# Optimization experiments

Hardware: AMD Instinct MI355X
Metric: run time of the kernel (lower is better)

## Reference

```python
import jax, jax.numpy as jnp
import numpy as np

B, S, F, H, P = 2048, 168, 7, 128, 96  # batch, window, features, hidden, pred_len


def setup_inputs() -> dict:
    key = jax.random.key(0)
    ks = jax.random.split(key, 16)
    sc = 0.05
    return {
        "xb": jax.random.normal(ks[0], (B, S, F), dtype=jnp.float32),
        # encoder LSTM (1 layer, unidirectional); gate order i,f,g,o like torch
        "W_ih_enc": jax.random.normal(ks[1], (4 * H, F), dtype=jnp.float32) * sc,
        "W_hh_enc": jax.random.normal(ks[2], (4 * H, H), dtype=jnp.float32) * sc,
        "b_ih_enc": jax.random.normal(ks[3], (4 * H,), dtype=jnp.float32) * sc,
        "b_hh_enc": jax.random.normal(ks[4], (4 * H,), dtype=jnp.float32) * sc,
        # attention linear: (H+F) -> S
        "W_att": jax.random.normal(ks[5], (S, H + F), dtype=jnp.float32) * sc,
        "b_att": jax.random.normal(ks[6], (S,), dtype=jnp.float32) * sc,
        # decoder LSTMCell: input_size=H, hidden=H
        "W_ih_dec": jax.random.normal(ks[7], (4 * H, H), dtype=jnp.float32) * sc,
        "W_hh_dec": jax.random.normal(ks[8], (4 * H, H), dtype=jnp.float32) * sc,
        "b_ih_dec": jax.random.normal(ks[9], (4 * H,), dtype=jnp.float32) * sc,
        "b_hh_dec": jax.random.normal(ks[10], (4 * H,), dtype=jnp.float32) * sc,
        # out linear: H -> F
        "W_out": jax.random.normal(ks[11], (F, H), dtype=jnp.float32) * sc,
        "b_out": jax.random.normal(ks[12], (F,), dtype=jnp.float32) * sc,
        # final linear (output_size==1 branch): F -> 1
        "W_fin": jax.random.normal(ks[13], (1, F), dtype=jnp.float32) * sc,
        "b_fin": jax.random.normal(ks[14], (1,), dtype=jnp.float32) * sc,
    }


def _gates(pre):
    i, f, g, o = jnp.split(pre, 4, axis=-1)
    return jax.nn.sigmoid(i), jax.nn.sigmoid(f), jnp.tanh(g), jax.nn.sigmoid(o)


def _forward(xb, W_ih_enc, W_hh_enc, b_ih_enc, b_hh_enc, W_att, b_att,
             W_ih_dec, W_hh_dec, b_ih_dec, b_hh_dec, W_out, b_out, W_fin, b_fin):
    b_enc = b_ih_enc + b_hh_enc
    x_ih = jnp.einsum('bsf,gf->sbg', xb, W_ih_enc)  # precompute input projections [S,B,4H]

    def enc_step(carry, xg):
        h, c = carry
        i, f, g, o = _gates(xg + h @ W_hh_enc.T + b_enc)
        c = f * c + i * g
        h = o * jnp.tanh(c)
        return (h, c), h

    h0 = jnp.zeros((xb.shape[0], W_hh_enc.shape[1]), dtype=xb.dtype)
    (h_T, _), enc_hs = jax.lax.scan(enc_step, (h0, h0), x_ih)
    encoder_output = jnp.transpose(enc_hs, (1, 0, 2))  # [B,S,H]

    b_dec = b_ih_dec + b_hh_dec

    def dec_step(carry, _):
        prev_h, y_prev = carry
        attn_in = jnp.concatenate([prev_h, y_prev], axis=1)          # [B,H+F]
        attn_w = jax.nn.softmax(attn_in @ W_att.T + b_att, axis=-1)  # [B,S]
        combine = jnp.einsum('bs,bsh->bh', attn_w, encoder_output)   # [B,H]
        # torch code: rnn_hidden, rnn_hidden = cell(combine, (prev_h, prev_h))
        # -> the CELL state c' is what survives; h'/output gate discarded.
        i, f, g, _ = _gates(combine @ W_ih_dec.T + prev_h @ W_hh_dec.T + b_dec)
        c_new = f * prev_h + i * g
        out = c_new @ W_out.T + b_out                                # [B,F]
        return (c_new, out), out

    y0 = xb[:, -1, :]
    _, outs = jax.lax.scan(dec_step, (h_T, y0), None, length=P)      # [P,B,F]
    outputs = jnp.transpose(outs, (1, 0, 2))                         # [B,P,F]
    return outputs @ W_fin.T + b_fin                                 # [B,P,1]


def reference(xb, W_ih_enc, W_hh_enc, b_ih_enc, b_hh_enc, W_att, b_att,
              W_ih_dec, W_hh_dec, b_ih_dec, b_hh_dec, W_out, b_out, W_fin, b_fin):
    return _forward(xb, W_ih_enc, W_hh_enc, b_ih_enc, b_hh_enc, W_att, b_att,
                    W_ih_dec, W_hh_dec, b_ih_dec, b_hh_dec, W_out, b_out, W_fin, b_fin)
```

## Files before the change

### kernel.cpp

```cpp
#include <hip/hip_runtime.h>
#include <hip/hip_fp8.h>

#define NB   2048
#define SEQ  168
#define NF   7
#define NH   128
#define NP   96
#define EROWS 8
#define DROWS 8
#define NTHR 512
#define KE   160
#define KD   256
#define HXS  168
#define CTS  264
#define LS4  30

typedef _Float16 h16;
typedef _Float16 h16x8 __attribute__((ext_vector_type(8)));
typedef float    f32x2 __attribute__((ext_vector_type(2)));
typedef float    f32x4 __attribute__((ext_vector_type(4)));
typedef unsigned int u32x4 __attribute__((ext_vector_type(4)));

__device__ __forceinline__ void mfma_av(f32x4& acc, h16x8 a, const h16x8& b_agpr) {
  asm("v_mfma_f32_16x16x32_f16 %0, %1, %2, %0"
      : "+v"(acc) : "v"(a), "a"(b_agpr));
}
#define PIN_A(x) asm volatile("" : "+a"(x))

__device__ __forceinline__ float sigm(float x) { return 1.f / (1.f + __expf(-x)); }
__device__ __forceinline__ float tanh_(float x) {
  float e = __expf(-2.f * fabsf(x));
  return copysignf((1.f - e) / (1.f + e), x);
}

template <bool HI>
__device__ __forceinline__ unsigned int pack2_fp8(float a, float b, unsigned int old) {
#if __has_builtin(__builtin_amdgcn_cvt_pk_fp8_f32)
  return (unsigned int)__builtin_amdgcn_cvt_pk_fp8_f32(a, b, (int)old, HI);
#else
  __hip_fp8_e4m3 qa(a), qb(b);
  unsigned int pair = (unsigned int)(*(unsigned char*)&qa) |
                      ((unsigned int)(*(unsigned char*)&qb) << 8);
  return HI ? ((old & 0x0000ffffu) | (pair << 16)) : ((old & 0xffff0000u) | pair);
#endif
}
template <bool HI>
__device__ __forceinline__ f32x2 unp2(unsigned int w) {
#if __has_builtin(__builtin_amdgcn_cvt_pk_f32_fp8)
  return __builtin_amdgcn_cvt_pk_f32_fp8(w, HI);
#else
  __hip_fp8_e4m3 a, b;
  constexpr unsigned int sh = HI ? 16 : 0;
  *(unsigned char*)&a = (w >> sh) & 0xff;
  *(unsigned char*)&b = (w >> (sh + 8)) & 0xff;
  f32x2 r; r.x = (float)a; r.y = (float)b; return r;
#endif
}

constexpr size_t WENC_OFF   = 0;
constexpr size_t WDEC_OFF   = 163840;
constexpr size_t WEFF_OFF   = 425984;
constexpr size_t BEFF_OFF   = 468992;
constexpr size_t WCOMB_OFF  = 469760;
constexpr size_t BCONST_OFF = 470272;
constexpr size_t BENC_OFF   = 470528;
constexpr size_t BDEC_OFF   = 472576;
constexpr size_t ENC_OFF    = 524288;
constexpr size_t ENC2_OFF   = 31981568;
constexpr size_t HT_OFF     = 44564480;

constexpr int HIST_OFF = 0;
constexpr int CATH_OFF = 122880;
constexpr int ATTW_OFF = 131328;
constexpr int WAT2_OFF = 136704;
constexpr int D0_OFF   = 146944;
constexpr int OUTP_OFF = 152320;
constexpr int YH_OFF   = 152576;
constexpr int DSMEM    = 152832;

__global__ void setup_weights(const float* __restrict__ Wih_enc, const float* __restrict__ Whh_enc,
                              const float* __restrict__ Wih_dec, const float* __restrict__ Whh_dec,
                              const float* __restrict__ Watt, const float* __restrict__ batt,
                              const float* __restrict__ Wout, const float* __restrict__ bout,
                              const float* __restrict__ Wfin, const float* __restrict__ bfin,
                              const float* __restrict__ bihe, const float* __restrict__ bhhe,
                              const float* __restrict__ bihd, const float* __restrict__ bhhd,
                              char* __restrict__ ws) {
  int idx = blockIdx.x * blockDim.x + threadIdx.x;
  constexpr int A0 = 81920;
  constexpr int A1 = A0 + 131072;
  constexpr int A2 = A1 + 21504;
  constexpr int A3 = A2 + 168;
  constexpr int A4 = A3 + 128;
  constexpr int A5 = A4 + 1;
  constexpr int A6 = A5 + 512;
  if (idx < A0) {
    int n = idx / KE, k = idx % KE;
    float v = 0.f;
    if (k < NF) v = Wih_enc[n * NF + k];
    else if (k >= 8 && k < 136) v = Whh_enc[n * NH + (k - 8)];
    ((h16*)(ws + WENC_OFF))[idx] = (h16)v;
  } else if (idx < A1) {
    int i = idx - A0;
    int n = i / KD, k = i % KD;
    float v = (k < NH) ? Wih_dec[n * NH + k] : Whh_dec[n * NH + (k - NH)];
    ((h16*)(ws + WDEC_OFF))[i] = (h16)v;
  } else if (idx < A2) {
    int i = idx - A1;
    int s = i / NH, k = i % NH;
    float v = Watt[s * (NH + NF) + k];
    #pragma unroll
    for (int f = 0; f < NF; ++f)
      v += Watt[s * (NH + NF) + NH + f] * Wout[f * NH + k];
    ((h16*)(ws + WEFF_OFF))[i] = (h16)v;
  } else if (idx < A3) {
    int s = idx - A2;
    float v = batt[s];
    #pragma unroll
    for (int f = 0; f < NF; ++f)
      v += Watt[s * (NH + NF) + NH + f] * bout[f];
    ((float*)(ws + BEFF_OFF))[s] = v;
  } else if (idx < A4) {
    int k = idx - A3;
    float v = 0.f;
    #pragma unroll
    for (int f = 0; f < NF; ++f) v += Wfin[f] * Wout[f * NH + k];
    ((float*)(ws + WCOMB_OFF))[k] = v;
  } else if (idx < A5) {
    float v = bfin[0];
    #pragma unroll
    for (int f = 0; f < NF; ++f) v += bout[f] * Wfin[f];
    ((float*)(ws + BCONST_OFF))[0] = v;
  } else if (idx < A6) {
    int g = idx - A5;
    ((float*)(ws + BENC_OFF))[g] = bihe[g] + bhhe[g];
    ((float*)(ws + BDEC_OFF))[g] = bihd[g] + bhhd[g];
  }
}

__global__ __attribute__((amdgpu_flat_work_group_size(NTHR, NTHR), amdgpu_waves_per_eu(2, 2)))
void enc_kernel(const float* __restrict__ xb, const h16* __restrict__ w16enc,
                const float* __restrict__ bencp, unsigned int* __restrict__ encw,
                unsigned int* __restrict__ encw2, float* __restrict__ hT) {
  __shared__ alignas(16) h16 sh_hx[2][16][HXS];

  const int t  = threadIdx.x;
  const int r0 = blockIdx.x * EROWS;

  for (int i = t; i < 2 * 16 * HXS; i += NTHR) ((h16*)sh_hx)[i] = (h16)0.f;
  __syncthreads();
  if (t < EROWS * NF) {
    int r = t / NF, f = t - (t / NF) * NF;
    sh_hx[0][r][f] = (h16)xb[((size_t)(r0 + r) * SEQ + 0) * NF + f];
  }

  const int w  = t >> 6;
  const int l  = t & 63;
  const int lq = l >> 4;
  const int ln = l & 15;
  const int hcol = w * 16 + ln;
  const int mrow = lq * 4;
  const bool act = (lq < 2);

  const int j  = t & 3;
  const int rf = t >> 2;
  const int xr = rf / NF;
  const int xf = rf - xr * NF;

  h16x8 bfE[4][5];
  float bE[4];
  #pragma unroll
  for (int g = 0; g < 4; ++g) {
    int n = g * 128 + hcol;
    bE[g] = bencp[n];
    #pragma unroll
    for (int kt = 0; kt < 5; ++kt) {
      bfE[g][kt] = *(const h16x8*)(w16enc + n * KE + kt * 32 + lq * 8);
      PIN_A(bfE[g][kt]);
    }
  }

  float creg[4] = {0.f, 0.f, 0.f, 0.f};
  float hlast[4] = {0.f, 0.f, 0.f, 0.f};
  float hprev[4] = {0.f, 0.f, 0.f, 0.f};
  unsigned int hpack[4] = {0u, 0u, 0u, 0u};
  float xstash = 0.f;

  __syncthreads();

  for (int s = 0; s < SEQ; ++s) {
    const int cur = s & 1;
    if ((s & 3) == 0 && t < EROWS * NF * 4) {
      int sx = s + 1 + j;
      xstash = (sx < SEQ) ? xb[((size_t)(r0 + xr) * SEQ + sx) * NF + xf] : 0.f;
    }

    f32x4 ac[4] = {{0.f,0.f,0.f,0.f},{0.f,0.f,0.f,0.f},{0.f,0.f,0.f,0.f},{0.f,0.f,0.f,0.f}};
    #pragma unroll
    for (int kt = 0; kt < 5; ++kt) {
      h16x8 af = *(const h16x8*)(&sh_hx[cur][ln][kt * 32 + lq * 8]);
      #pragma unroll
      for (int g = 0; g < 4; ++g)
        mfma_av(ac[g], af, bfE[g][kt]);
    }

    if (act) {
      #pragma unroll
      for (int reg = 0; reg < 4; ++reg) {
        float gi = sigm(ac[0][reg] + bE[0]);
        float gf = sigm(ac[1][reg] + bE[1]);
        float gg = tanh_(ac[2][reg] + bE[2]);
        float go = sigm(ac[3][reg] + bE[3]);
        float c = gf * creg[reg] + gi * gg;
        creg[reg] = c;
        float h = go * tanh_(c);
        hlast[reg] = h;
        sh_hx[cur ^ 1][mrow + reg][8 + hcol] = (h16)h;
        float hs = h * 16.f;
        if ((s & 1) == 0) hprev[reg] = hs;
        else if ((s & 3) == 1) hpack[reg] = pack2_fp8<false>(hprev[reg], hs, hpack[reg]);
        else                   hpack[reg] = pack2_fp8<true>(hprev[reg], hs, hpack[reg]);
      }
      if ((s & 3) == 3) {
        int s4 = s >> 2;
        if (s4 < LS4) {
          #pragma unroll
          for (int reg = 0; reg < 4; ++reg)
            encw[((size_t)(r0 + mrow + reg) * LS4 + s4) * NH + hcol] = hpack[reg];
        } else {
          int q = s4 - LS4;
          #pragma unroll
          for (int reg = 0; reg < 4; ++reg)
            encw2[(((size_t)(r0 + mrow + reg) * 3 + (q >> 2)) * NH + hcol) * 4 + (q & 3)] = hpack[reg];
        }
      }
    }
    if (t < EROWS * NF * 4 && (s & 3) == j && s + 1 < SEQ)
      sh_hx[cur ^ 1][xr][xf] = (h16)xstash;
    __syncthreads();
  }

  if (act) {
    #pragma unroll
    for (int reg = 0; reg < 4; ++reg)
      hT[(size_t)(r0 + mrow + reg) * NH + hcol] = hlast[reg];
  }
}

__global__ __attribute__((amdgpu_flat_work_group_size(NTHR, NTHR), amdgpu_waves_per_eu(2, 2)))
void dec_kernel(const float* __restrict__ xb, const float* __restrict__ Watt,
                const float* __restrict__ Wout, const float* __restrict__ bout,
                const h16* __restrict__ w16dec, const h16* __restrict__ weff,
                const float* __restrict__ beffp, const float* __restrict__ wcombp,
                const float* __restrict__ bconstp, const float* __restrict__ bdecp,
                const unsigned int* __restrict__ encw, const unsigned int* __restrict__ encw2,
                const float* __restrict__ hT, float* __restrict__ out) {
  extern __shared__ char smem[];
  unsigned int* hist = (unsigned int*)(smem + HIST_OFF);
  h16*   sh_cath  = (h16*)(smem + CATH_OFF);
  float* sh_attw  = (float*)(smem + ATTW_OFF);
  h16*   sh_watt2 = (h16*)(smem + WAT2_OFF);
  float* sh_d0    = (float*)(smem + D0_OFF);
  float* sh_outp  = (float*)(smem + OUTP_OFF);
  float* sh_yh    = (float*)(smem + YH_OFF);

  const int t  = threadIdx.x;
  const int r0 = blockIdx.x * DROWS;

  for (int i = t; i < 2 * 8 * CTS; i += NTHR)   sh_cath[i] = (h16)0.f;
  for (int i = t; i < 40 * NH; i += NTHR)       sh_watt2[i] = weff[128 * NH + i];
  {
    const u32x4* src = (const u32x4*)(encw + (size_t)r0 * LS4 * NH);
    for (int i = t; i < (DROWS * LS4 * NH) / 4; i += NTHR)
      ((u32x4*)hist)[i] = src[i];
  }

  const int w  = t >> 6;
  const int l  = t & 63;
  const int lq = l >> 4;
  const int ln = l & 15;
  const int hcol = w * 16 + ln;
  const bool act = (lq < 2);

  h16x8 bfD[3][8];
  float bD[3];
  #pragma unroll
  for (int g = 0; g < 3; ++g) {
    int n = g * 128 + hcol;
    bD[g] = bdecp[n];
    #pragma unroll
    for (int kt = 0; kt < 8; ++kt) {
      bfD[g][kt] = *(const h16x8*)(w16dec + n * KD + kt * 32 + lq * 8);
      PIN_A(bfD[g][kt]);
    }
  }
  h16x8 bfA[4];
  #pragma unroll
  for (int kt = 0; kt < 4; ++kt) {
    bfA[kt] = *(const h16x8*)(weff + hcol * NH + kt * 32 + lq * 8);
    PIN_A(bfA[kt]);
  }
  const float beffR = beffp[hcol];
  const int s2v = 128 + hcol;
  const float beff2 = (w < 3 && s2v < SEQ) ? beffp[s2v] : 0.f;
  const float wcombR = wcombp[hcol];
  const float bconstv = bconstp[0];

  float creg[4] = {0.f, 0.f, 0.f, 0.f};
  if (act) {
    #pragma unroll
    for (int reg = 0; reg < 4; ++reg) {
      int row = lq * 4 + reg;
      float hv = hT[(size_t)(r0 + row) * NH + hcol];
      creg[reg] = hv;
      sh_cath[0 * 8 * CTS + row * CTS + 128 + hcol] = (h16)hv;
    }
  }
  if (t < DROWS * NF) {
    int r = t / NF, f = t - (t / NF) * NF;
    float a = bout[f];
    const float* wr = Wout + f * NH;
    const float* hp = hT + (size_t)(r0 + r) * NH;
    #pragma unroll 8
    for (int k = 0; k < NH; k += 4) {
      float4 pv = *(const float4*)(hp + k);
      float4 wv = *(const float4*)(wr + k);
      a += pv.x * wv.x + pv.y * wv.y + pv.z * wv.z + pv.w * wv.w;
    }
    sh_yh[t] = a;
  }
  __syncthreads();
  for (int i = t; i < DROWS * SEQ; i += NTHR) {
    int r = i / SEQ, s = i - (i / SEQ) * SEQ;
    float a = 0.f;
    #pragma unroll
    for (int f = 0; f < NF; ++f) {
      float y0f = xb[((size_t)(r0 + r) * SEQ + (SEQ - 1)) * NF + f];
      a += (y0f - sh_yh[r * NF + f]) * Watt[s * (NH + NF) + NH + f];
    }
    sh_d0[i] = a;
  }

  const int dr = t >> 7;
  const int dh = t & 127;
  const unsigned int* hrowA = hist + (size_t)dr * (LS4 * NH) + dh;
  const unsigned int* hrowB = hist + (size_t)(dr + 4) * (LS4 * NH) + dh;
  const float* erowA = sh_attw + dr * SEQ;
  const float* erowB = sh_attw + (dr + 4) * SEQ;

  u32x4 tA[3], tB[3];
  {
    const u32x4* e2 = (const u32x4*)encw2;
    #pragma unroll
    for (int b = 0; b < 3; ++b) {
      tA[b] = e2[((size_t)(r0 + dr)     * 3 + b) * NH + dh];
      tB[b] = e2[((size_t)(r0 + dr + 4) * 3 + b) * NH + dh];
    }
  }
  __syncthreads();

  for (int p = 0; p < NP; ++p) {
    const int CA = p & 1;

    if (p > 0 && t < DROWS) {
      float a = bconstv;
      #pragma unroll
      for (int w2 = 0; w2 < 8; ++w2) a += sh_outp[w2 * 8 + t];
      out[(size_t)(r0 + t) * NP + (p - 1)] = a;
    }

    {
      h16x8 afA[4];
      #pragma unroll
      for (int kt = 0; kt < 4; ++kt)
        afA[kt] = *(const h16x8*)(sh_cath + CA * 8 * CTS + (ln & 7) * CTS + 128 + kt * 32 + lq * 8);
      f32x4 acc = {0.f, 0.f, 0.f, 0.f};
      #pragma unroll
      for (int kt = 0; kt < 4; ++kt)
        mfma_av(acc, afA[kt], bfA[kt]);
      if (act) {
        #pragma unroll
        for (int reg = 0; reg < 4; ++reg) {
          int row = lq * 4 + reg;
          float lg = acc[reg] + beffR;
          if (p == 0) lg += sh_d0[row * SEQ + hcol];
          lg = fminf(fmaxf(lg, -30.f), 30.f);
          sh_attw[row * SEQ + hcol] = __expf(lg);
        }
      }
      if (w < 3) {
        int srow = (s2v < SEQ ? s2v : SEQ - 1) - 128;
        f32x4 acc2 = {0.f, 0.f, 0.f, 0.f};
        #pragma unroll
        for (int kt = 0; kt < 4; ++kt) {
          h16x8 bf2 = *(const h16x8*)(sh_watt2 + srow * NH + kt * 32 + lq * 8);
          acc2 = __builtin_amdgcn_mfma_f32_16x16x32_f16(afA[kt], bf2, acc2, 0, 0, 0);
        }
        if (s2v < SEQ && act) {
          #pragma unroll
          for (int reg = 0; reg < 4; ++reg) {
            int row = lq * 4 + reg;
            float lg = acc2[reg] + beff2;
            if (p == 0) lg += sh_d0[row * SEQ + s2v];
            lg = fminf(fmaxf(lg, -30.f), 30.f);
            sh_attw[row * SEQ + s2v] = __expf(lg);
          }
        }
      }
    }
    __syncthreads();

    {
      float dA = erowA[l] + erowA[64 + l];
      float dB = erowB[l] + erowB[64 + l];
      if (l < SEQ - 128) { dA += erowA[128 + l]; dB += erowB[128 + l]; }
      #pragma unroll
      for (int k = 1; k < 64; k <<= 1) {
        dA += __shfl_xor(dA, k);
        dB += __shfl_xor(dB, k);
      }
      const float invA = 0.0625f / dA;
      const float invB = 0.0625f / dB;

      f32x2 avA = {0.f, 0.f};
      f32x2 avB = {0.f, 0.f};
      #pragma unroll 6
      for (int s4 = 0; s4 < LS4; ++s4) {
        unsigned int evA = hrowA[s4 * NH];
        unsigned int evB = hrowB[s4 * NH];
        float4 eA = *(const float4*)(erowA + s4 * 4);
        float4 eB = *(const float4*)(erowB + s4 * 4);
        f32x2 wA01 = {eA.x, eA.y}, wA23 = {eA.z, eA.w};
        f32x2 wB01 = {eB.x, eB.y}, wB23 = {eB.z, eB.w};
        avA = wA01 * unp2<false>(evA) + avA;
        avA = wA23 * unp2<true>(evA) + avA;
        avB = wB01 * unp2<false>(evB) + avB;
        avB = wB23 * unp2<true>(evB) + avB;
      }
      #pragma unroll
      for (int b = 0; b < 3; ++b) {
        #pragma unroll
        for (int jj = 0; jj < 4; ++jj) {
          int s4 = LS4 + b * 4 + jj;
          unsigned int evA = tA[b][jj];
          unsigned int evB = tB[b][jj];
          float4 eA = *(const float4*)(erowA + s4 * 4);
          float4 eB = *(const float4*)(erowB + s4 * 4);
          f32x2 wA01 = {eA.x, eA.y}, wA23 = {eA.z, eA.w};
          f32x2 wB01 = {eB.x, eB.y}, wB23 = {eB.z, eB.w};
          avA = wA01 * unp2<false>(evA) + avA;
          avA = wA23 * unp2<true>(evA) + avA;
          avB = wB01 * unp2<false>(evB) + avB;
          avB = wB23 * unp2<true>(evB) + avB;
        }
      }
      sh_cath[CA * 8 * CTS + dr * CTS + dh]       = (h16)((avA.x + avA.y) * invA);
      sh_cath[CA * 8 * CTS + (dr + 4) * CTS + dh] = (h16)((avB.x + avB.y) * invB);
    }
    __syncthreads();

    {
      f32x4 ag[3] = {{0.f,0.f,0.f,0.f},{0.f,0.f,0.f,0.f},{0.f,0.f,0.f,0.f}};
      #pragma unroll
      for (int kt = 0; kt < 8; ++kt) {
        h16x8 af = *(const h16x8*)(sh_cath + CA * 8 * CTS + (ln & 7) * CTS + kt * 32 + lq * 8);
        #pragma unroll
        for (int g = 0; g < 3; ++g)
          mfma_av(ag[g], af, bfD[g][kt]);
      }
      if (act) {
        float contrib[4];
        #pragma unroll
        for (int reg = 0; reg < 4; ++reg) {
          int row = lq * 4 + reg;
          float gi = sigm(ag[0][reg] + bD[0]);
          float gf = sigm(ag[1][reg] + bD[1]);
          float gg = tanh_(ag[2][reg] + bD[2]);
          float cn = gf * creg[reg] + gi * gg;
          creg[reg] = cn;
          sh_cath[(CA ^ 1) * 8 * CTS + row * CTS + 128 + hcol] = (h16)cn;
          contrib[reg] = cn * wcombR;
        }
        #pragma unroll
        for (int reg = 0; reg < 4; ++reg) {
          float rsum = contrib[reg];
          rsum += __shfl_xor(rsum, 1);
          rsum += __shfl_xor(rsum, 2);
          rsum += __shfl_xor(rsum, 4);
          rsum += __shfl_xor(rsum, 8);
          if (ln == 0) sh_outp[w * 8 + lq * 4 + reg] = rsum;
        }
      }
    }
    __syncthreads();
  }

  if (t < DROWS) {
    float a = bconstv;
    #pragma unroll
    for (int w2 = 0; w2 < 8; ++w2) a += sh_outp[w2 * 8 + t];
    out[(size_t)(r0 + t) * NP + (NP - 1)] = a;
  }
}

extern "C" void kernel_launch(void* const* d_in, const int* in_sizes, int n_in,
                              void* d_out, int out_size, void* d_ws, size_t ws_size,
                              hipStream_t stream) {
  const float* xb      = (const float*)d_in[0];
  const float* Wih_enc = (const float*)d_in[1];
  const float* Whh_enc = (const float*)d_in[2];
  const float* bih_enc = (const float*)d_in[3];
  const float* bhh_enc = (const float*)d_in[4];
  const float* Watt    = (const float*)d_in[5];
  const float* batt    = (const float*)d_in[6];
  const float* Wih_dec = (const float*)d_in[7];
  const float* Whh_dec = (const float*)d_in[8];
  const float* bih_dec = (const float*)d_in[9];
  const float* bhh_dec = (const float*)d_in[10];
  const float* Wout    = (const float*)d_in[11];
  const float* bout    = (const float*)d_in[12];
  const float* Wfin    = (const float*)d_in[13];
  const float* bfin    = (const float*)d_in[14];
  char* ws = (char*)d_ws;

  hipFuncSetAttribute(reinterpret_cast<const void*>(dec_kernel),
                      hipFuncAttributeMaxDynamicSharedMemorySize, DSMEM);

  setup_weights<<<920, 256, 0, stream>>>(Wih_enc, Whh_enc, Wih_dec, Whh_dec,
                                         Watt, batt, Wout, bout, Wfin, bfin,
                                         bih_enc, bhh_enc, bih_dec, bhh_dec, ws);
  enc_kernel<<<NB / EROWS, NTHR, 0, stream>>>(
      xb, (const h16*)(ws + WENC_OFF), (const float*)(ws + BENC_OFF),
      (unsigned int*)(ws + ENC_OFF), (unsigned int*)(ws + ENC2_OFF),
      (float*)(ws + HT_OFF));
  dec_kernel<<<NB / DROWS, NTHR, DSMEM, stream>>>(
      xb, Watt, Wout, bout,
      (const h16*)(ws + WDEC_OFF), (const h16*)(ws + WEFF_OFF),
      (const float*)(ws + BEFF_OFF), (const float*)(ws + WCOMB_OFF),
      (const float*)(ws + BCONST_OFF), (const float*)(ws + BDEC_OFF),
      (const unsigned int*)(ws + ENC_OFF), (const unsigned int*)(ws + ENC2_OFF),
      (const float*)(ws + HT_OFF), (float*)d_out);
}
```

Measured before the change: 929.1 us.

## Fuse encoder and decoder into one kernel with LDS-resident encoder history

Merges the encoder and decoder kernels into a single kernel per 8-row block. Encoder history is written straight into shared memory instead of a global buffer that the decoder re-reads, and x is preloaded into LDS as fp16. The decoder's hidden-state matmul now runs early, overlapping the attention computation. Softmax denominators come from per-wave partial sums instead of a cross-lane reduction over exp values, and outputs are buffered eight steps at a time before being written. The cost is larger shared memory for the encoder phase, which may lower occupancy, and a longer serial kernel.

```diff
diff --git a/kernel.cpp b/kernel.cpp
--- a/kernel.cpp
+++ b/kernel.cpp
@@ -65,18 +65,22 @@
 constexpr size_t BCONST_OFF = 470272;
 constexpr size_t BENC_OFF   = 470528;
 constexpr size_t BDEC_OFF   = 472576;
-constexpr size_t ENC_OFF    = 524288;
 constexpr size_t ENC2_OFF   = 31981568;
 constexpr size_t HT_OFF     = 44564480;
 
-constexpr int HIST_OFF = 0;
-constexpr int CATH_OFF = 122880;
-constexpr int ATTW_OFF = 131328;
-constexpr int WAT2_OFF = 136704;
-constexpr int D0_OFF   = 146944;
-constexpr int OUTP_OFF = 152320;
-constexpr int YH_OFF   = 152576;
-constexpr int DSMEM    = 152832;
+constexpr int HIST_OFF   = 0;
+constexpr int CATH_OFF   = 122880;
+constexpr int ATTW_OFF   = 131328;
+constexpr int WAT2_OFF   = 136704;
+constexpr int D0_OFF     = 146944;
+constexpr int OUTP_OFF   = 152320;
+constexpr int YH_OFF     = 152576;
+constexpr int DPART_OFF  = 152832;
+constexpr int DPART2_OFF = 153088;
+constexpr int OBUF_OFF   = 153216;
+constexpr int DSMEM      = 153472;
+constexpr int SHHX_OFF = 122880;
+constexpr int X16_OFF  = 133632;
 
 __global__ void setup_weights(const float* __restrict__ Wih_enc, const float* __restrict__ Whh_enc,
                               const float* __restrict__ Wih_dec, const float* __restrict__ Whh_dec,
@@ -139,20 +143,31 @@
 }
 
 __global__ __attribute__((amdgpu_flat_work_group_size(NTHR, NTHR), amdgpu_waves_per_eu(2, 2)))
-void enc_kernel(const float* __restrict__ xb, const h16* __restrict__ w16enc,
-                const float* __restrict__ bencp, unsigned int* __restrict__ encw,
-                unsigned int* __restrict__ encw2, float* __restrict__ hT) {
-  __shared__ alignas(16) h16 sh_hx[2][16][HXS];
+void fused_kernel(const float* __restrict__ xb, const h16* __restrict__ w16enc,
+                  const float* __restrict__ bencp, unsigned int* __restrict__ encw2,
+                  float* __restrict__ hTg,
+                  const float* __restrict__ Watt, const float* __restrict__ Wout,
+                  const float* __restrict__ bout,
+                  const h16* __restrict__ w16dec, const h16* __restrict__ weff,
+                  const float* __restrict__ beffp, const float* __restrict__ wcombp,
+                  const float* __restrict__ bconstp, const float* __restrict__ bdecp,
+                  float* __restrict__ out) {
+  extern __shared__ char smem[];
+  unsigned int* hist = (unsigned int*)(smem + HIST_OFF);
+  h16 (*sh_hx)[16][HXS] = (h16(*)[16][HXS])(smem + SHHX_OFF);
+  h16*   x16      = (h16*)(smem + X16_OFF);
+  h16*   sh_cath  = (h16*)(smem + CATH_OFF);
+  float* sh_attw  = (float*)(smem + ATTW_OFF);
+  h16*   sh_watt2 = (h16*)(smem + WAT2_OFF);
+  float* sh_d0    = (float*)(smem + D0_OFF);
+  float* sh_outp  = (float*)(smem + OUTP_OFF);
+  float* sh_yh    = (float*)(smem + YH_OFF);
+  float* sh_dp    = (float*)(smem + DPART_OFF);
+  float* sh_dp2   = (float*)(smem + DPART2_OFF);
+  float* sh_obuf  = (float*)(smem + OBUF_OFF);
 
   const int t  = threadIdx.x;
   const int r0 = blockIdx.x * EROWS;
-
-  for (int i = t; i < 2 * 16 * HXS; i += NTHR) ((h16*)sh_hx)[i] = (h16)0.f;
-  __syncthreads();
-  if (t < EROWS * NF) {
-    int r = t / NF, f = t - (t / NF) * NF;
-    sh_hx[0][r][f] = (h16)xb[((size_t)(r0 + r) * SEQ + 0) * NF + f];
-  }
 
   const int w  = t >> 6;
   const int l  = t & 63;
@@ -162,10 +177,9 @@
   const int mrow = lq * 4;
   const bool act = (lq < 2);
 
-  const int j  = t & 3;
-  const int rf = t >> 2;
-  const int xr = rf / NF;
-  const int xf = rf - xr * NF;
+  for (int i = t; i < 2 * 16 * HXS; i += NTHR) ((h16*)sh_hx)[i] = (h16)0.f;
+  for (int i = t; i < EROWS * SEQ * NF; i += NTHR)
+    x16[i] = (h16)xb[(size_t)r0 * SEQ * NF + i];
 
   h16x8 bfE[4][5];
   float bE[4];
@@ -179,21 +193,21 @@
       PIN_A(bfE[g][kt]);
     }
   }
+  __syncthreads();
+  if (t < EROWS * NF) {
+    int r = t / NF, f = t - (t / NF) * NF;
+    sh_hx[0][r][f] = x16[(r * SEQ + 0) * NF + f];
+  }
 
   float creg[4] = {0.f, 0.f, 0.f, 0.f};
-  float hlast[4] = {0.f, 0.f, 0.f, 0.f};
+  float hstate[4] = {0.f, 0.f, 0.f, 0.f};
   float hprev[4] = {0.f, 0.f, 0.f, 0.f};
   unsigned int hpack[4] = {0u, 0u, 0u, 0u};
-  float xstash = 0.f;
 
   __syncthreads();
 
   for (int s = 0; s < SEQ; ++s) {
     const int cur = s & 1;
-    if ((s & 3) == 0 && t < EROWS * NF * 4) {
-      int sx = s + 1 + j;
-      xstash = (sx < SEQ) ? xb[((size_t)(r0 + xr) * SEQ + sx) * NF + xf] : 0.f;
-    }
 
     f32x4 ac[4] = {{0.f,0.f,0.f,0.f},{0.f,0.f,0.f,0.f},{0.f,0.f,0.f,0.f},{0.f,0.f,0.f,0.f}};
     #pragma unroll
@@ -214,7 +228,7 @@
         float c = gf * creg[reg] + gi * gg;
         creg[reg] = c;
         float h = go * tanh_(c);
-        hlast[reg] = h;
+        hstate[reg] = h;
         sh_hx[cur ^ 1][mrow + reg][8 + hcol] = (h16)h;
         float hs = h * 16.f;
         if ((s & 1) == 0) hprev[reg] = hs;
@@ -226,7 +240,7 @@
         if (s4 < LS4) {
           #pragma unroll
           for (int reg = 0; reg < 4; ++reg)
-            encw[((size_t)(r0 + mrow + reg) * LS4 + s4) * NH + hcol] = hpack[reg];
+            hist[(size_t)(mrow + reg) * (LS4 * NH) + s4 * NH + hcol] = hpack[reg];
         } else {
           int q = s4 - LS4;
           #pragma unroll
@@ -235,52 +249,23 @@
         }
       }
     }
-    if (t < EROWS * NF * 4 && (s & 3) == j && s + 1 < SEQ)
-      sh_hx[cur ^ 1][xr][xf] = (h16)xstash;
+    if (t < EROWS * NF && s + 1 < SEQ) {
+      int r = t / NF, f = t - (t / NF) * NF;
+      sh_hx[cur ^ 1][r][f] = x16[(r * SEQ + (s + 1)) * NF + f];
+    }
     __syncthreads();
   }
 
   if (act) {
     #pragma unroll
     for (int reg = 0; reg < 4; ++reg)
-      hT[(size_t)(r0 + mrow + reg) * NH + hcol] = hlast[reg];
-  }
-}
-
-__global__ __attribute__((amdgpu_flat_work_group_size(NTHR, NTHR), amdgpu_waves_per_eu(2, 2)))
-void dec_kernel(const float* __restrict__ xb, const float* __restrict__ Watt,
-                const float* __restrict__ Wout, const float* __restrict__ bout,
-                const h16* __restrict__ w16dec, const h16* __restrict__ weff,
-                const float* __restrict__ beffp, const float* __restrict__ wcombp,
-                const float* __restrict__ bconstp, const float* __restrict__ bdecp,
-                const unsigned int* __restrict__ encw, const unsigned int* __restrict__ encw2,
-                const float* __restrict__ hT, float* __restrict__ out) {
-  extern __shared__ char smem[];
-  unsigned int* hist = (unsigned int*)(smem + HIST_OFF);
-  h16*   sh_cath  = (h16*)(smem + CATH_OFF);
-  float* sh_attw  = (float*)(smem + ATTW_OFF);
-  h16*   sh_watt2 = (h16*)(smem + WAT2_OFF);
-  float* sh_d0    = (float*)(smem + D0_OFF);
-  float* sh_outp  = (float*)(smem + OUTP_OFF);
-  float* sh_yh    = (float*)(smem + YH_OFF);
-
-  const int t  = threadIdx.x;
-  const int r0 = blockIdx.x * DROWS;
-
-  for (int i = t; i < 2 * 8 * CTS; i += NTHR)   sh_cath[i] = (h16)0.f;
-  for (int i = t; i < 40 * NH; i += NTHR)       sh_watt2[i] = weff[128 * NH + i];
-  {
-    const u32x4* src = (const u32x4*)(encw + (size_t)r0 * LS4 * NH);
-    for (int i = t; i < (DROWS * LS4 * NH) / 4; i += NTHR)
-      ((u32x4*)hist)[i] = src[i];
-  }
-
-  const int w  = t >> 6;
-  const int l  = t & 63;
-  const int lq = l >> 4;
-  const int ln = l & 15;
-  const int hcol = w * 16 + ln;
-  const bool act = (lq < 2);
+      hTg[(size_t)(r0 + mrow + reg) * NH + hcol] = hstate[reg];
+  }
+  __builtin_amdgcn_sched_barrier(0);
+  __syncthreads();
+
+  for (int i = t; i < 40 * NH; i += NTHR) sh_watt2[i] = weff[128 * NH + i];
+  if (t < 32) sh_dp2[t] = 0.f;
 
   h16x8 bfD[3][8];
   float bD[3];
@@ -306,21 +291,18 @@
   const float wcombR = wcombp[hcol];
   const float bconstv = bconstp[0];
 
-  float creg[4] = {0.f, 0.f, 0.f, 0.f};
   if (act) {
     #pragma unroll
     for (int reg = 0; reg < 4; ++reg) {
-      int row = lq * 4 + reg;
-      float hv = hT[(size_t)(r0 + row) * NH + hcol];
-      creg[reg] = hv;
-      sh_cath[0 * 8 * CTS + row * CTS + 128 + hcol] = (h16)hv;
+      creg[reg] = hstate[reg];
+      sh_cath[0 * 8 * CTS + (mrow + reg) * CTS + 128 + hcol] = (h16)hstate[reg];
     }
   }
   if (t < DROWS * NF) {
     int r = t / NF, f = t - (t / NF) * NF;
     float a = bout[f];
     const float* wr = Wout + f * NH;
-    const float* hp = hT + (size_t)(r0 + r) * NH;
+    const float* hp = hTg + (size_t)(r0 + r) * NH;
     #pragma unroll 8
     for (int k = 0; k < NH; k += 4) {
       float4 pv = *(const float4*)(hp + k);
@@ -359,6 +341,8 @@
   }
   __syncthreads();
 
+  f32x4 aghh[3];
+
   for (int p = 0; p < NP; ++p) {
     const int CA = p & 1;
 
@@ -366,7 +350,14 @@
       float a = bconstv;
       #pragma unroll
       for (int w2 = 0; w2 < 8; ++w2) a += sh_outp[w2 * 8 + t];
-      out[(size_t)(r0 + t) * NP + (p - 1)] = a;
+      int slot = (p - 1) & 7;
+      sh_obuf[t * 8 + slot] = a;
+      if (slot == 7) {
+        int base = p - 8;
+        #pragma unroll
+        for (int j = 0; j < 8; ++j)
+          out[(size_t)(r0 + t) * NP + base + j] = sh_obuf[t * 8 + j];
+      }
     }
 
     {
@@ -378,14 +369,34 @@
       #pragma unroll
       for (int kt = 0; kt < 4; ++kt)
         mfma_av(acc, afA[kt], bfA[kt]);
+      #pragma unroll
+      for (int g = 0; g < 3; ++g) {
+        f32x4 z = {0.f, 0.f, 0.f, 0.f};
+        aghh[g] = z;
+        #pragma unroll
+        for (int kt = 0; kt < 4; ++kt)
+          mfma_av(aghh[g], afA[kt], bfD[g][4 + kt]);
+      }
+
+      float ev[4];
       if (act) {
         #pragma unroll
         for (int reg = 0; reg < 4; ++reg) {
-          int row = lq * 4 + reg;
+          int row = mrow + reg;
           float lg = acc[reg] + beffR;
           if (p == 0) lg += sh_d0[row * SEQ + hcol];
           lg = fminf(fmaxf(lg, -30.f), 30.f);
-          sh_attw[row * SEQ + hcol] = __expf(lg);
+          ev[reg] = __expf(lg);
+          sh_attw[row * SEQ + hcol] = ev[reg];
+        }
+        #pragma unroll
+        for (int reg = 0; reg < 4; ++reg) {
+          float rs = ev[reg];
+          rs += __shfl_xor(rs, 1);
+          rs += __shfl_xor(rs, 2);
+          rs += __shfl_xor(rs, 4);
+          rs += __shfl_xor(rs, 8);
+          if (ln == 0) sh_dp[(mrow + reg) * 8 + w] = rs;
         }
       }
       if (w < 3) {
@@ -396,29 +407,46 @@
           h16x8 bf2 = *(const h16x8*)(sh_watt2 + srow * NH + kt * 32 + lq * 8);
           acc2 = __builtin_amdgcn_mfma_f32_16x16x32_f16(afA[kt], bf2, acc2, 0, 0, 0);
         }
-        if (s2v < SEQ && act) {
+        if (act) {
+          float ev2[4];
           #pragma unroll
           for (int reg = 0; reg < 4; ++reg) {
-            int row = lq * 4 + reg;
-            float lg = acc2[reg] + beff2;
-            if (p == 0) lg += sh_d0[row * SEQ + s2v];
-            lg = fminf(fmaxf(lg, -30.f), 30.f);
-            sh_attw[row * SEQ + s2v] = __expf(lg);
+            int row = mrow + reg;
+            float e2v = 0.f;
+            if (s2v < SEQ) {
+              float lg = acc2[reg] + beff2;
+              if (p == 0) lg += sh_d0[row * SEQ + s2v];
+              lg = fminf(fmaxf(lg, -30.f), 30.f);
+              e2v = __expf(lg);
+              sh_attw[row * SEQ + s2v] = e2v;
+            }
+            ev2[reg] = e2v;
           }
+          #pragma unroll
+          for (int reg = 0; reg < 4; ++reg) {
+            float rs = ev2[reg];
+            rs += __shfl_xor(rs, 1);
+            rs += __shfl_xor(rs, 2);
+            rs += __shfl_xor(rs, 4);
+            rs += __shfl_xor(rs, 8);
+            if (ln == 0) sh_dp2[(mrow + reg) * 4 + w] = rs;
+          }
         }
       }
     }
     __syncthreads();
 
     {
-      float dA = erowA[l] + erowA[64 + l];
-      float dB = erowB[l] + erowB[64 + l];
-      if (l < SEQ - 128) { dA += erowA[128 + l]; dB += erowB[128 + l]; }
-      #pragma unroll
-      for (int k = 1; k < 64; k <<= 1) {
-        dA += __shfl_xor(dA, k);
-        dB += __shfl_xor(dB, k);
-      }
+      float4 qa0 = *(const float4*)(sh_dp + dr * 8);
+      float4 qa1 = *(const float4*)(sh_dp + dr * 8 + 4);
+      float4 qa2 = *(const float4*)(sh_dp2 + dr * 4);
+      float4 qb0 = *(const float4*)(sh_dp + (dr + 4) * 8);
+      float4 qb1 = *(const float4*)(sh_dp + (dr + 4) * 8 + 4);
+      float4 qb2 = *(const float4*)(sh_dp2 + (dr + 4) * 4);
+      float dA = ((qa0.x + qa0.y) + (qa0.z + qa0.w)) + ((qa1.x + qa1.y) + (qa1.z + qa1.w))
+               + ((qa2.x + qa2.y) + (qa2.z + qa2.w));
+      float dB = ((qb0.x + qb0.y) + (qb0.z + qb0.w)) + ((qb1.x + qb1.y) + (qb1.z + qb1.w))
+               + ((qb2.x + qb2.y) + (qb2.z + qb2.w));
       const float invA = 0.0625f / dA;
       const float invB = 0.0625f / dB;
 
@@ -460,9 +488,9 @@
     __syncthreads();
 
     {
-      f32x4 ag[3] = {{0.f,0.f,0.f,0.f},{0.f,0.f,0.f,0.f},{0.f,0.f,0.f,0.f}};
-      #pragma unroll
-      for (int kt = 0; kt < 8; ++kt) {
+      f32x4 ag[3] = {aghh[0], aghh[1], aghh[2]};
+      #pragma unroll
+      for (int kt = 0; kt < 4; ++kt) {
         h16x8 af = *(const h16x8*)(sh_cath + CA * 8 * CTS + (ln & 7) * CTS + kt * 32 + lq * 8);
         #pragma unroll
         for (int g = 0; g < 3; ++g)
@@ -472,7 +500,7 @@
         float contrib[4];
         #pragma unroll
         for (int reg = 0; reg < 4; ++reg) {
-          int row = lq * 4 + reg;
+          int row = mrow + reg;
           float gi = sigm(ag[0][reg] + bD[0]);
           float gf = sigm(ag[1][reg] + bD[1]);
           float gg = tanh_(ag[2][reg] + bD[2]);
@@ -488,7 +516,7 @@
           rsum += __shfl_xor(rsum, 2);
           rsum += __shfl_xor(rsum, 4);
           rsum += __shfl_xor(rsum, 8);
-          if (ln == 0) sh_outp[w * 8 + lq * 4 + reg] = rsum;
+          if (ln == 0) sh_outp[w * 8 + mrow + reg] = rsum;
         }
       }
     }
@@ -499,7 +527,10 @@
     float a = bconstv;
     #pragma unroll
     for (int w2 = 0; w2 < 8; ++w2) a += sh_outp[w2 * 8 + t];
-    out[(size_t)(r0 + t) * NP + (NP - 1)] = a;
+    sh_obuf[t * 8 + 7] = a;
+    #pragma unroll
+    for (int j = 0; j < 8; ++j)
+      out[(size_t)(r0 + t) * NP + (NP - 8) + j] = sh_obuf[t * 8 + j];
   }
 }
 
@@ -523,21 +554,18 @@
   const float* bfin    = (const float*)d_in[14];
   char* ws = (char*)d_ws;
 
-  hipFuncSetAttribute(reinterpret_cast<const void*>(dec_kernel),
+  hipFuncSetAttribute(reinterpret_cast<const void*>(fused_kernel),
                       hipFuncAttributeMaxDynamicSharedMemorySize, DSMEM);
 
   setup_weights<<<920, 256, 0, stream>>>(Wih_enc, Whh_enc, Wih_dec, Whh_dec,
                                          Watt, batt, Wout, bout, Wfin, bfin,
                                          bih_enc, bhh_enc, bih_dec, bhh_dec, ws);
-  enc_kernel<<<NB / EROWS, NTHR, 0, stream>>>(
+  fused_kernel<<<NB / EROWS, NTHR, DSMEM, stream>>>(
       xb, (const h16*)(ws + WENC_OFF), (const float*)(ws + BENC_OFF),
-      (unsigned int*)(ws + ENC_OFF), (unsigned int*)(ws + ENC2_OFF),
-      (float*)(ws + HT_OFF));
-  dec_kernel<<<NB / DROWS, NTHR, DSMEM, stream>>>(
-      xb, Watt, Wout, bout,
+      (unsigned int*)(ws + ENC2_OFF), (float*)(ws + HT_OFF),
+      Watt, Wout, bout,
       (const h16*)(ws + WDEC_OFF), (const h16*)(ws + WEFF_OFF),
       (const float*)(ws + BEFF_OFF), (const float*)(ws + WCOMB_OFF),
       (const float*)(ws + BCONST_OFF), (const float*)(ws + BDEC_OFF),
-      (const unsigned int*)(ws + ENC_OFF), (const unsigned int*)(ws + ENC2_OFF),
-      (const float*)(ws + HT_OFF), (float*)d_out);
-}
+      (float*)d_out);
+}
```

After: 996.0 us. 7.2% more time.
